# Kernel tuning notes

Hardware: AMD Instinct MI355X
Metric: run time of the kernel (lower is better)

## Reference

```python
import math
import jax, jax.numpy as jnp
import numpy as np

DIM = 512
HEADS = 8
LS = 64  # local_size
SCALE = (DIM // HEADS) ** -0.5


def _normalize(x, eps=1e-12):
    # torch F.normalize(dim=-1): x / max(||x||, eps)
    n = jnp.linalg.norm(x, axis=-1, keepdims=True)
    return x / jnp.maximum(n, eps)


def setup_inputs() -> dict:
    key = jax.random.key(0)
    k0, k1, k2 = jax.random.split(key, 3)
    B, S, D = 8, 4096, DIM
    return {
        "x": jax.random.normal(k0, (B, S, D), jnp.float32),
        "W_qkv": jax.random.normal(k1, (D, 3 * D), jnp.float32) * 0.02,
        "b_qkv": jnp.zeros((3 * D,), jnp.float32),
        "W_proj": jax.random.normal(k2, (D, D), jnp.float32) * 0.02,
        "b_proj": jnp.zeros((D,), jnp.float32),
    }


def reference(x, W_qkv, b_qkv, W_proj, b_proj):
    B, S, D = x.shape
    H = HEADS
    d = D // H
    ls = LS
    nl = S // ls
    ntimes = int(math.log2(nl))

    # qkv projection -> [3, B, H, S, d]
    qkv = (x @ W_qkv + b_qkv).reshape(B, S, 3, H, d).transpose(2, 0, 3, 1, 4)
    q_pre = qkv[0].reshape(B * H, S, d).transpose(0, 2, 1)  # [BH, d, S]

    q_idx_last = jnp.broadcast_to(jnp.arange(S)[None, :], (B * H, S))

    # recursive content-based bipartition (unrolled: ntimes is static)
    for _ in range(ntimes):
        bh, dd, n = q_pre.shape
        q_avg = q_pre.reshape(bh, dd, 2, n // 2).mean(-1)        # [bh, d, 2]
        q_avg = _normalize(q_avg.transpose(0, 2, 1))             # [bh, 2, d]
        q_norm = _normalize(q_pre.transpose(0, 2, 1))            # [bh, n, d]
        # squared euclidean distance [bh, n, 2]
        sq = (jnp.sum(q_norm ** 2, -1)[:, :, None]
              + jnp.sum(q_avg ** 2, -1)[:, None, :]
              - 2.0 * jnp.einsum('bnd,bcd->bnc', q_norm, q_avg))
        q_ratio = (sq[:, :, 0] + 1.0) / (sq[:, :, 1] + 1.0)
        q_idx = jnp.argsort(q_ratio, axis=-1)                    # [bh, n]
        q_idx_last = jnp.take_along_axis(q_idx_last, q_idx, axis=-1).reshape(bh * 2, n // 2)
        q_pre = jnp.take_along_axis(q_pre, q_idx[:, None, :], axis=-1)
        # 'b d (c n) -> (b c) d n' with c=2
        q_pre = q_pre.reshape(bh, dd, 2, n // 2).transpose(0, 2, 1, 3).reshape(bh * 2, dd, n // 2)

    q_idx = q_idx_last.reshape(B, H, S)
    q_idx_rev = jnp.argsort(q_idx, axis=-1)

    # gather qkv along token dim with routed permutation
    qkv_pre = jnp.take_along_axis(qkv, q_idx[None, :, :, :, None], axis=3)  # [3,B,H,S,d]
    # 'qkv b h (nl ls) d -> qkv (b nl) h ls d'
    qkv_pre = qkv_pre.reshape(3, B, H, nl, ls, d).transpose(0, 1, 3, 2, 4, 5).reshape(3, B * nl, H, ls, d)
    q, k, v = qkv_pre[0], qkv_pre[1], qkv_pre[2]

    # windowed diff-softmax-mul attention (softmax over head dim d)
    attn = jax.nn.softmax((q - k) * SCALE, axis=-1)
    out = attn * v                                               # [(B nl), H, ls, d]

    # '(b nl) h ls d -> b h d (nl ls)'
    out = out.reshape(B, nl, H, ls, d).transpose(0, 2, 4, 1, 3).reshape(B, H, d, S)
    out = jnp.take_along_axis(out, q_idx_rev[:, :, None, :], axis=-1)
    res = out.reshape(B, D, S).transpose(0, 2, 1)                # [B, S, D]
    res = res @ W_proj + b_proj
    return x + res
```

## Files before the change

kernel.cpp:

```cpp
#include <hip/hip_runtime.h>
#include <hip/hip_bf16.h>

typedef __bf16 bf16;
typedef __attribute__((ext_vector_type(8))) __bf16 bf16x8;
typedef __attribute__((ext_vector_type(4))) __bf16 bf16x4;
typedef __attribute__((ext_vector_type(4))) float f32x4;

#define M_TOK 32768
#define D_    512
#define N_QKV 1536
#define BK    64
#define SCALE_ 0.125f

#define AS1 __attribute__((address_space(1)))
#define AS3 __attribute__((address_space(3)))

__global__ __launch_bounds__(256) void cvt_bf16(const float* __restrict__ in,
                                                bf16* __restrict__ out, int n4) {
  int i = blockIdx.x * 256 + threadIdx.x;
  if (i >= n4) return;
  f32x4 v = ((const f32x4*)in)[i];
  bf16x4 o;
  o[0] = (bf16)v[0]; o[1] = (bf16)v[1]; o[2] = (bf16)v[2]; o[3] = (bf16)v[3];
  ((bf16x4*)out)[i] = o;
}

template <int PERM>
__global__ __launch_bounds__(256) void transpose_cvt(const float* __restrict__ in,
                                                     bf16* __restrict__ out,
                                                     int K, int N) {
  __shared__ float tile[32][33];
  int n0 = blockIdx.x * 32, k0 = blockIdx.y * 32;
  int tx = threadIdx.x, ty = threadIdx.y;
  for (int i = 0; i < 32; i += 8)
    tile[ty + i][tx] = in[(size_t)(k0 + ty + i) * N + n0 + tx];
  __syncthreads();
  for (int i = 0; i < 32; i += 8) {
    int n = n0 + ty + i;
    int np = n;
    if (PERM) {
      int qkv = n >> 9, h = (n & 511) >> 6, c = n & 63;
      np = h * 192 + (c >> 5) * 96 + qkv * 32 + (c & 31);
    }
    out[(size_t)np * K + k0 + tx] = (bf16)tile[tx][ty + i];
  }
}

__global__ __launch_bounds__(256, 2) void gemm_qkv_softmax(const bf16* __restrict__ A,
                                                           const bf16* __restrict__ Bt,
                                                           const float* __restrict__ bqkv,
                                                           bf16* __restrict__ O) {
  __shared__ __align__(16) bf16 sA[2][128 * BK];
  __shared__ __align__(16) bf16 sB[2][192 * BK];

  const int tid = threadIdx.x;
  const int w = tid >> 6;
  const int l = tid & 63;
  const int m0 = blockIdx.x * 128;
  const int h  = blockIdx.y;
  const int n0 = h * 192;
  const int wrow = w >> 1, wcol = w & 1;

  f32x4 acc[4][6];
#pragma unroll
  for (int i = 0; i < 4; ++i)
#pragma unroll
    for (int j = 0; j < 6; ++j) {
      f32x4 z = {0.f, 0.f, 0.f, 0.f};
      acc[i][j] = z;
    }

  const int srow = l >> 3;
  const int schunk = ((l & 7) ^ (l >> 3)) * 8;

  const int fr = l & 15;
  const int fkc = l >> 4;
  const int frs = fr & 7;

  const bf16* gA = A + (size_t)(m0 + w * 32 + srow) * D_ + schunk;
  const bf16* gB = Bt + (size_t)(n0 + w * 48 + srow) * D_ + schunk;

  auto stageA = [&](int buf, int kt) {
#pragma unroll
    for (int q = 0; q < 4; ++q)
      __builtin_amdgcn_global_load_lds((AS1 const void*)(gA + (size_t)(q * 8) * D_ + kt),
                                       (AS3 void*)&sA[buf][(w * 32 + q * 8) * BK], 16, 0, 0);
  };
  auto stageB = [&](int buf, int kt) {
#pragma unroll
    for (int q = 0; q < 6; ++q)
      __builtin_amdgcn_global_load_lds((AS1 const void*)(gB + (size_t)(q * 8) * D_ + kt),
                                       (AS3 void*)&sB[buf][(w * 48 + q * 8) * BK], 16, 0, 0);
  };

  auto compute = [&](int buf, int kk) {
    const int sw = (((kk << 2) | fkc) ^ frs) * 8;
    bf16x8 af[4], bfr[6];
#pragma unroll
    for (int i = 0; i < 4; ++i)
      af[i] = *(const bf16x8*)&sA[buf][(wrow * 64 + i * 16 + fr) * BK + sw];
#pragma unroll
    for (int j = 0; j < 6; ++j)
      bfr[j] = *(const bf16x8*)&sB[buf][(wcol * 96 + j * 16 + fr) * BK + sw];
    __builtin_amdgcn_s_setprio(1);
#pragma unroll
    for (int i = 0; i < 4; ++i)
#pragma unroll
      for (int j = 0; j < 6; ++j)
        acc[i][j] = __builtin_amdgcn_mfma_f32_16x16x32_bf16(af[i], bfr[j], acc[i][j], 0, 0, 0);
    __builtin_amdgcn_s_setprio(0);
  };

  stageA(0, 0);
  stageB(0, 0);

  const int NT = D_ / BK;
  for (int t = 0; t < NT - 1; ++t) {
    const int cur = t & 1;
    stageA(cur ^ 1, (t + 1) * BK);
    asm volatile("s_waitcnt vmcnt(4)" ::: "memory");
    __builtin_amdgcn_s_barrier();
    asm volatile("" ::: "memory");
    compute(cur, 0);
    stageB(cur ^ 1, (t + 1) * BK);
    compute(cur, 1);
    asm volatile("" ::: "memory");
    __builtin_amdgcn_s_barrier();
  }
  {
    const int cur = (NT - 1) & 1;
    asm volatile("s_waitcnt vmcnt(0)" ::: "memory");
    __builtin_amdgcn_s_barrier();
    asm volatile("" ::: "memory");
    compute(cur, 0);
    compute(cur, 1);
    asm volatile("" ::: "memory");
    __builtin_amdgcn_s_barrier();
  }

  float bq[2], bkk[2], bv[2];
#pragma unroll
  for (int jq = 0; jq < 2; ++jq) {
    int c = h * 64 + wcol * 32 + jq * 16 + fr;
    bq[jq]  = bqkv[c];
    bkk[jq] = bqkv[512 + c];
    bv[jq]  = bqkv[1024 + c];
  }

  float* xm = (float*)&sA[0][0];
  float* xs = xm + 256;
  const int rbase = (l >> 4) * 4;

  float mpart[4][4], spart[4][4];
#pragma unroll
  for (int i = 0; i < 4; ++i) {
#pragma unroll
    for (int r = 0; r < 4; ++r) {
      float s0 = (acc[i][0][r] + bq[0] - acc[i][2][r] - bkk[0]) * SCALE_;
      float s1 = (acc[i][1][r] + bq[1] - acc[i][3][r] - bkk[1]) * SCALE_;
      float mx = fmaxf(s0, s1);
#pragma unroll
      for (int off = 1; off < 16; off <<= 1) mx = fmaxf(mx, __shfl_xor(mx, off));
      float e0 = __expf(s0 - mx);
      float e1 = __expf(s1 - mx);
      acc[i][0][r] = e0;
      acc[i][1][r] = e1;
      float sm = e0 + e1;
#pragma unroll
      for (int off = 1; off < 16; off <<= 1) sm += __shfl_xor(sm, off);
      mpart[i][r] = mx;
      spart[i][r] = sm;
      if (fr == 0) {
        int row = wrow * 64 + i * 16 + rbase + r;
        xm[wcol * 128 + row] = mx;
        xs[wcol * 128 + row] = sm;
      }
    }
  }
  __syncthreads();

#pragma unroll
  for (int i = 0; i < 4; ++i) {
#pragma unroll
    for (int r = 0; r < 4; ++r) {
      int row = wrow * 64 + i * 16 + rbase + r;
      float mo = xm[(wcol ^ 1) * 128 + row];
      float so = xs[(wcol ^ 1) * 128 + row];
      float mx = mpart[i][r];
      float M  = fmaxf(mx, mo);
      float esc_self  = __expf(mx - M);
      float esc_other = __expf(mo - M);
      float total = spart[i][r] * esc_self + so * esc_other;
      float inv = esc_self / total;
      int m = m0 + row;
      float o0 = acc[i][0][r] * inv * (acc[i][4][r] + bv[0]);
      float o1 = acc[i][1][r] * inv * (acc[i][5][r] + bv[1]);
      O[(size_t)m * D_ + h * 64 + wcol * 32 + fr]      = (bf16)o0;
      O[(size_t)m * D_ + h * 64 + wcol * 32 + 16 + fr] = (bf16)o1;
    }
  }
}

__global__ __launch_bounds__(256, 2) void gemm_bt_f32(const bf16* __restrict__ A,
                                                      const bf16* __restrict__ Bt,
                                                      const float* __restrict__ bias,
                                                      const float* __restrict__ resid,
                                                      float* __restrict__ C,
                                                      int M, int N, int K) {
  __shared__ __align__(16) bf16 sA[2][128 * BK];
  __shared__ __align__(16) bf16 sB[2][128 * BK];

  const int tid = threadIdx.x;
  const int w = tid >> 6;
  const int l = tid & 63;
  const int m0 = blockIdx.x * 128;
  const int n0 = blockIdx.y * 128;
  const int wrow = w >> 1, wcol = w & 1;

  f32x4 acc[4][4];
#pragma unroll
  for (int i = 0; i < 4; ++i)
#pragma unroll
    for (int j = 0; j < 4; ++j) {
      f32x4 z = {0.f, 0.f, 0.f, 0.f};
      acc[i][j] = z;
    }

  const int srow = l >> 3;
  const int schunk = ((l & 7) ^ (l >> 3)) * 8;
  const int fr = l & 15;
  const int fkc = l >> 4;
  const int frs = fr & 7;

  const bf16* gA = A + (size_t)(m0 + w * 32 + srow) * K + schunk;
  const bf16* gB = Bt + (size_t)(n0 + w * 32 + srow) * K + schunk;

  auto stageA = [&](int buf, int kt) {
#pragma unroll
    for (int q = 0; q < 4; ++q)
      __builtin_amdgcn_global_load_lds((AS1 const void*)(gA + (size_t)(q * 8) * K + kt),
                                       (AS3 void*)&sA[buf][(w * 32 + q * 8) * BK], 16, 0, 0);
  };
  auto stageB = [&](int buf, int kt) {
#pragma unroll
    for (int q = 0; q < 4; ++q)
      __builtin_amdgcn_global_load_lds((AS1 const void*)(gB + (size_t)(q * 8) * K + kt),
                                       (AS3 void*)&sB[buf][(w * 32 + q * 8) * BK], 16, 0, 0);
  };

  auto compute = [&](int buf, int kk) {
    const int sw = (((kk << 2) | fkc) ^ frs) * 8;
    bf16x8 af[4], bfr[4];
#pragma unroll
    for (int i = 0; i < 4; ++i)
      af[i] = *(const bf16x8*)&sA[buf][(wrow * 64 + i * 16 + fr) * BK + sw];
#pragma unroll
    for (int j = 0; j < 4; ++j)
      bfr[j] = *(const bf16x8*)&sB[buf][(wcol * 64 + j * 16 + fr) * BK + sw];
    __builtin_amdgcn_s_setprio(1);
#pragma unroll
    for (int i = 0; i < 4; ++i)
#pragma unroll
      for (int j = 0; j < 4; ++j)
        acc[i][j] = __builtin_amdgcn_mfma_f32_16x16x32_bf16(af[i], bfr[j], acc[i][j], 0, 0, 0);
    __builtin_amdgcn_s_setprio(0);
  };

  stageA(0, 0);
  stageB(0, 0);

  const int nt = K / BK;
  for (int t = 0; t < nt - 1; ++t) {
    const int cur = t & 1;
    stageA(cur ^ 1, (t + 1) * BK);
    asm volatile("s_waitcnt vmcnt(4)" ::: "memory");
    __builtin_amdgcn_s_barrier();
    asm volatile("" ::: "memory");
    compute(cur, 0);
    stageB(cur ^ 1, (t + 1) * BK);
    compute(cur, 1);
    asm volatile("" ::: "memory");
    __builtin_amdgcn_s_barrier();
  }
  {
    const int cur = (nt - 1) & 1;
    asm volatile("s_waitcnt vmcnt(0)" ::: "memory");
    __builtin_amdgcn_s_barrier();
    asm volatile("" ::: "memory");
    compute(cur, 0);
    compute(cur, 1);
  }

  const int col = l & 15;
  const int rbase = (l >> 4) * 4;
#pragma unroll
  for (int j = 0; j < 4; ++j) {
    int n = n0 + wcol * 64 + j * 16 + col;
    float bv = bias[n];
#pragma unroll
    for (int i = 0; i < 4; ++i) {
#pragma unroll
      for (int r = 0; r < 4; ++r) {
        int m = m0 + wrow * 64 + i * 16 + rbase + r;
        C[(size_t)m * N + n] = acc[i][j][r] + bv + resid[(size_t)m * N + n];
      }
    }
  }
}

extern "C" void kernel_launch(void* const* d_in, const int* in_sizes, int n_in,
                              void* d_out, int out_size, void* d_ws, size_t ws_size,
                              hipStream_t stream) {
  const float* x     = (const float*)d_in[0];
  const float* Wqkv  = (const float*)d_in[1];
  const float* bqkv  = (const float*)d_in[2];
  const float* Wproj = (const float*)d_in[3];
  const float* bproj = (const float*)d_in[4];
  float* out = (float*)d_out;

  char* ws = (char*)d_ws;
  bf16* Wq_t = (bf16*)ws;
  bf16* Wp_t = (bf16*)(ws + (size_t)N_QKV * D_ * 2);
  char* p = ws + (size_t)N_QKV * D_ * 2 + (size_t)D_ * D_ * 2;
  bf16* Xb = (bf16*)p;
  bf16* O  = (bf16*)(p + (size_t)M_TOK * D_ * 2);

  transpose_cvt<1><<<dim3(N_QKV / 32, D_ / 32), dim3(32, 8), 0, stream>>>(Wqkv, Wq_t, D_, N_QKV);
  transpose_cvt<0><<<dim3(D_ / 32, D_ / 32), dim3(32, 8), 0, stream>>>(Wproj, Wp_t, D_, D_);

  cvt_bf16<<<(M_TOK * D_ / 4 + 255) / 256, 256, 0, stream>>>(x, Xb, M_TOK * D_ / 4);

  gemm_qkv_softmax<<<dim3(M_TOK / 128, 8), 256, 0, stream>>>(Xb, Wq_t, bqkv, O);

  gemm_bt_f32<<<dim3(M_TOK / 128, D_ / 128), 256, 0, stream>>>(
      O, Wp_t, bproj, x, out, M_TOK, D_, D_);
}
```

Measured before the change: 238.2 us.

## Enlarge QKV GEMM tile to 256 rows with 8 waves and triple-buffered A

The fused QKV+softmax GEMM now uses 512-thread blocks covering 256 token rows. The A operand is triple-buffered and B double-buffered, and the k-loop is rewritten into four phases per tile. Global-to-LDS prefetches are interleaved between MFMA groups, with explicit lgkmcnt waits and sched barriers. This aims to reuse each B tile across more rows and hide load latency better. In exchange it uses more LDS per block, which may reduce occupancy, and adds more barriers per k-step.

Measured after the change: 245.2 us. +2.9%, slower.

```diff
diff --git a/kernel.cpp b/kernel.cpp
--- a/kernel.cpp
+++ b/kernel.cpp
@@ -46,17 +46,17 @@
   }
 }
 
-__global__ __launch_bounds__(256, 2) void gemm_qkv_softmax(const bf16* __restrict__ A,
+__global__ __launch_bounds__(512, 2) void gemm_qkv_softmax(const bf16* __restrict__ A,
                                                            const bf16* __restrict__ Bt,
                                                            const float* __restrict__ bqkv,
                                                            bf16* __restrict__ O) {
-  __shared__ __align__(16) bf16 sA[2][128 * BK];
+  __shared__ __align__(16) bf16 sA[3][256 * BK];
   __shared__ __align__(16) bf16 sB[2][192 * BK];
 
   const int tid = threadIdx.x;
   const int w = tid >> 6;
   const int l = tid & 63;
-  const int m0 = blockIdx.x * 128;
+  const int m0 = blockIdx.x * 256;
   const int h  = blockIdx.y;
   const int n0 = h * 192;
   const int wrow = w >> 1, wcol = w & 1;
@@ -78,63 +78,95 @@
   const int frs = fr & 7;
 
   const bf16* gA = A + (size_t)(m0 + w * 32 + srow) * D_ + schunk;
-  const bf16* gB = Bt + (size_t)(n0 + w * 48 + srow) * D_ + schunk;
-
-  auto stageA = [&](int buf, int kt) {
-#pragma unroll
-    for (int q = 0; q < 4; ++q)
-      __builtin_amdgcn_global_load_lds((AS1 const void*)(gA + (size_t)(q * 8) * D_ + kt),
-                                       (AS3 void*)&sA[buf][(w * 32 + q * 8) * BK], 16, 0, 0);
-  };
-  auto stageB = [&](int buf, int kt) {
-#pragma unroll
-    for (int q = 0; q < 6; ++q)
-      __builtin_amdgcn_global_load_lds((AS1 const void*)(gB + (size_t)(q * 8) * D_ + kt),
-                                       (AS3 void*)&sB[buf][(w * 48 + q * 8) * BK], 16, 0, 0);
-  };
-
-  auto compute = [&](int buf, int kk) {
+  const bf16* gB = Bt + (size_t)(n0 + w * 24 + srow) * D_ + schunk;
+
+  auto stA = [&](int buf, int kt, int q) {
+    __builtin_amdgcn_global_load_lds((AS1 const void*)(gA + (size_t)(q * 8) * D_ + kt),
+                                     (AS3 void*)&sA[buf][(w * 32 + q * 8) * BK], 16, 0, 0);
+  };
+  auto stB = [&](int buf, int kt, int q) {
+    __builtin_amdgcn_global_load_lds((AS1 const void*)(gB + (size_t)(q * 8) * D_ + kt),
+                                     (AS3 void*)&sB[buf][(w * 24 + q * 8) * BK], 16, 0, 0);
+  };
+
+  bf16x8 af[4];
+  auto loadA = [&](int buf, int kk) {
     const int sw = (((kk << 2) | fkc) ^ frs) * 8;
-    bf16x8 af[4], bfr[6];
 #pragma unroll
     for (int i = 0; i < 4; ++i)
       af[i] = *(const bf16x8*)&sA[buf][(wrow * 64 + i * 16 + fr) * BK + sw];
-#pragma unroll
-    for (int j = 0; j < 6; ++j)
-      bfr[j] = *(const bf16x8*)&sB[buf][(wcol * 96 + j * 16 + fr) * BK + sw];
+  };
+  bf16x8 bfr[3];
+  auto loadB3 = [&](int buf, int kk, int jh) {
+    const int sw = (((kk << 2) | fkc) ^ frs) * 8;
+#pragma unroll
+    for (int j = 0; j < 3; ++j)
+      bfr[j] = *(const bf16x8*)&sB[buf][(wcol * 96 + (jh * 3 + j) * 16 + fr) * BK + sw];
+  };
+  auto mfma12 = [&](int jh) {
     __builtin_amdgcn_s_setprio(1);
 #pragma unroll
     for (int i = 0; i < 4; ++i)
 #pragma unroll
-      for (int j = 0; j < 6; ++j)
-        acc[i][j] = __builtin_amdgcn_mfma_f32_16x16x32_bf16(af[i], bfr[j], acc[i][j], 0, 0, 0);
+      for (int j = 0; j < 3; ++j)
+        acc[i][jh * 3 + j] =
+            __builtin_amdgcn_mfma_f32_16x16x32_bf16(af[i], bfr[j], acc[i][jh * 3 + j], 0, 0, 0);
     __builtin_amdgcn_s_setprio(0);
   };
 
-  stageA(0, 0);
-  stageB(0, 0);
+#pragma unroll
+  for (int q = 0; q < 4; ++q) stA(0, 0, q);
+#pragma unroll
+  for (int q = 0; q < 3; ++q) stB(0, 0, q);
+#pragma unroll
+  for (int q = 0; q < 4; ++q) stA(1, BK, q);
 
   const int NT = D_ / BK;
-  for (int t = 0; t < NT - 1; ++t) {
-    const int cur = t & 1;
-    stageA(cur ^ 1, (t + 1) * BK);
-    asm volatile("s_waitcnt vmcnt(4)" ::: "memory");
-    __builtin_amdgcn_s_barrier();
-    asm volatile("" ::: "memory");
-    compute(cur, 0);
-    stageB(cur ^ 1, (t + 1) * BK);
-    compute(cur, 1);
-    asm volatile("" ::: "memory");
-    __builtin_amdgcn_s_barrier();
-  }
-  {
-    const int cur = (NT - 1) & 1;
-    asm volatile("s_waitcnt vmcnt(0)" ::: "memory");
-    __builtin_amdgcn_s_barrier();
-    asm volatile("" ::: "memory");
-    compute(cur, 0);
-    compute(cur, 1);
-    asm volatile("" ::: "memory");
+#pragma unroll
+  for (int t = 0; t < NT; ++t) {
+    const int cA = t % 3;
+    const int cB = t & 1;
+    const int nA = (t + 2) % 3;
+    const int nB = cB ^ 1;
+    const int ktA = (t + 2) * BK;
+    const int ktB = (t + 1) * BK;
+    const bool pfA = (t < NT - 2);
+    const bool pfB = (t < NT - 1);
+
+    if (pfB) { stB(nB, ktB, 0); stB(nB, ktB, 1); }
+    if (t < NT - 1)
+      asm volatile("s_waitcnt vmcnt(6)" ::: "memory");
+    else
+      asm volatile("s_waitcnt vmcnt(0)" ::: "memory");
+    __builtin_amdgcn_s_barrier();
+    loadA(cA, 0);
+    loadB3(cB, 0, 0);
+    asm volatile("s_waitcnt lgkmcnt(0)" ::: "memory");
+    __builtin_amdgcn_sched_barrier(0);
+    mfma12(0);
+    __builtin_amdgcn_s_barrier();
+
+    loadB3(cB, 0, 1);
+    if (pfB) stB(nB, ktB, 2);
+    if (pfA) stA(nA, ktA, 0);
+    asm volatile("s_waitcnt lgkmcnt(0)" ::: "memory");
+    __builtin_amdgcn_sched_barrier(0);
+    mfma12(1);
+    __builtin_amdgcn_s_barrier();
+
+    loadA(cA, 1);
+    loadB3(cB, 1, 0);
+    if (pfA) { stA(nA, ktA, 1); stA(nA, ktA, 2); }
+    asm volatile("s_waitcnt lgkmcnt(0)" ::: "memory");
+    __builtin_amdgcn_sched_barrier(0);
+    mfma12(0);
+    __builtin_amdgcn_s_barrier();
+
+    loadB3(cB, 1, 1);
+    if (pfA) stA(nA, ktA, 3);
+    asm volatile("s_waitcnt lgkmcnt(0)" ::: "memory");
+    __builtin_amdgcn_sched_barrier(0);
+    mfma12(1);
     __builtin_amdgcn_s_barrier();
   }
 
@@ -148,7 +180,7 @@
   }
 
   float* xm = (float*)&sA[0][0];
-  float* xs = xm + 256;
+  float* xs = xm + 512;
   const int rbase = (l >> 4) * 4;
 
   float mpart[4][4], spart[4][4];
@@ -172,8 +204,8 @@
       spart[i][r] = sm;
       if (fr == 0) {
         int row = wrow * 64 + i * 16 + rbase + r;
-        xm[wcol * 128 + row] = mx;
-        xs[wcol * 128 + row] = sm;
+        xm[wcol * 256 + row] = mx;
+        xs[wcol * 256 + row] = sm;
       }
     }
   }
@@ -184,8 +216,8 @@
 #pragma unroll
     for (int r = 0; r < 4; ++r) {
       int row = wrow * 64 + i * 16 + rbase + r;
-      float mo = xm[(wcol ^ 1) * 128 + row];
-      float so = xs[(wcol ^ 1) * 128 + row];
+      float mo = xm[(wcol ^ 1) * 256 + row];
+      float so = xs[(wcol ^ 1) * 256 + row];
       float mx = mpart[i][r];
       float M  = fmaxf(mx, mo);
       float esc_self  = __expf(mx - M);
@@ -330,7 +362,7 @@
 
   cvt_bf16<<<(M_TOK * D_ / 4 + 255) / 256, 256, 0, stream>>>(x, Xb, M_TOK * D_ / 4);
 
-  gemm_qkv_softmax<<<dim3(M_TOK / 128, 8), 256, 0, stream>>>(Xb, Wq_t, bqkv, O);
+  gemm_qkv_softmax<<<dim3(M_TOK / 256, 8), 512, 0, stream>>>(Xb, Wq_t, bqkv, O);
 
   gemm_bt_f32<<<dim3(M_TOK / 128, D_ / 128), 256, 0, stream>>>(
       O, Wp_t, bproj, x, out, M_TOK, D_, D_);
```

## Fuse x fp32-to-bf16 conversion into QKV GEMM A-tile loading

Applied to the files above, without the earlier changes.

Removes the separate cvt_bf16 pass over x and has the QKV GEMM load fp32 x directly into registers, convert to bf16, and write it into swizzled LDS. The load/compute pipeline is restructured so next-tile A loads go to registers and B loads go straight to LDS, with the LDS write after compute. The two weight transpose kernels are merged into one launch. Cost: the GEMM reads x at twice the bytes, and the eight x tiles are re-read by each head block, so more HBM/L2 traffic and register pressure inside the GEMM.

New measurement: 229.6 us. 3.6% less time.

```diff
diff --git a/kernel.cpp b/kernel.cpp
--- a/kernel.cpp
+++ b/kernel.cpp
@@ -15,38 +15,35 @@
 #define AS1 __attribute__((address_space(1)))
 #define AS3 __attribute__((address_space(3)))
 
-__global__ __launch_bounds__(256) void cvt_bf16(const float* __restrict__ in,
-                                                bf16* __restrict__ out, int n4) {
-  int i = blockIdx.x * 256 + threadIdx.x;
-  if (i >= n4) return;
-  f32x4 v = ((const f32x4*)in)[i];
-  bf16x4 o;
-  o[0] = (bf16)v[0]; o[1] = (bf16)v[1]; o[2] = (bf16)v[2]; o[3] = (bf16)v[3];
-  ((bf16x4*)out)[i] = o;
-}
-
-template <int PERM>
-__global__ __launch_bounds__(256) void transpose_cvt(const float* __restrict__ in,
-                                                     bf16* __restrict__ out,
-                                                     int K, int N) {
+__global__ __launch_bounds__(256) void transpose_cvt_all(const float* __restrict__ Wqkv,
+                                                         const float* __restrict__ Wproj,
+                                                         bf16* __restrict__ Wq_t,
+                                                         bf16* __restrict__ Wp_t) {
   __shared__ float tile[32][33];
-  int n0 = blockIdx.x * 32, k0 = blockIdx.y * 32;
-  int tx = threadIdx.x, ty = threadIdx.y;
+  const int bx = blockIdx.x;
+  const float* in;
+  bf16* out;
+  int N, n0;
+  bool perm;
+  if (bx < 48) { in = Wqkv;  out = Wq_t; N = 1536; n0 = bx * 32;        perm = true;  }
+  else         { in = Wproj; out = Wp_t; N = 512;  n0 = (bx - 48) * 32; perm = false; }
+  const int k0 = blockIdx.y * 32;
+  const int tx = threadIdx.x, ty = threadIdx.y;
   for (int i = 0; i < 32; i += 8)
     tile[ty + i][tx] = in[(size_t)(k0 + ty + i) * N + n0 + tx];
   __syncthreads();
   for (int i = 0; i < 32; i += 8) {
     int n = n0 + ty + i;
     int np = n;
-    if (PERM) {
+    if (perm) {
       int qkv = n >> 9, h = (n & 511) >> 6, c = n & 63;
       np = h * 192 + (c >> 5) * 96 + qkv * 32 + (c & 31);
     }
-    out[(size_t)np * K + k0 + tx] = (bf16)tile[tx][ty + i];
+    out[(size_t)np * D_ + k0 + tx] = (bf16)tile[tx][ty + i];
   }
 }
 
-__global__ __launch_bounds__(256, 2) void gemm_qkv_softmax(const bf16* __restrict__ A,
+__global__ __launch_bounds__(256, 2) void gemm_qkv_softmax(const float* __restrict__ A,
                                                            const bf16* __restrict__ Bt,
                                                            const float* __restrict__ bqkv,
                                                            bf16* __restrict__ O) {
@@ -71,20 +68,31 @@
     }
 
   const int srow = l >> 3;
-  const int schunk = ((l & 7) ^ (l >> 3)) * 8;
-
+  const int schunk = ((l & 7) ^ srow) * 8;
   const int fr = l & 15;
   const int fkc = l >> 4;
   const int frs = fr & 7;
 
-  const bf16* gA = A + (size_t)(m0 + w * 32 + srow) * D_ + schunk;
-  const bf16* gB = Bt + (size_t)(n0 + w * 48 + srow) * D_ + schunk;
-
-  auto stageA = [&](int buf, int kt) {
-#pragma unroll
-    for (int q = 0; q < 4; ++q)
-      __builtin_amdgcn_global_load_lds((AS1 const void*)(gA + (size_t)(q * 8) * D_ + kt),
-                                       (AS3 void*)&sA[buf][(w * 32 + q * 8) * BK], 16, 0, 0);
+  const float* gA = A + (size_t)(m0 + w * 32 + srow) * D_ + (l & 7) * 8;
+  const bf16*  gB = Bt + (size_t)(n0 + w * 48 + srow) * D_ + schunk;
+
+  f32x4 areg[4][2];
+  auto aregLoad = [&](int kt) {
+#pragma unroll
+    for (int q = 0; q < 4; ++q) {
+      const float* gp = gA + (size_t)(q * 8) * D_ + kt;
+      areg[q][0] = *(const f32x4*)gp;
+      areg[q][1] = *(const f32x4*)(gp + 4);
+    }
+  };
+  auto aWrite = [&](int buf) {
+#pragma unroll
+    for (int q = 0; q < 4; ++q) {
+      bf16x8 v;
+#pragma unroll
+      for (int e = 0; e < 4; ++e) { v[e] = (bf16)areg[q][0][e]; v[4 + e] = (bf16)areg[q][1][e]; }
+      *(bf16x8*)&sA[buf][(w * 32 + q * 8 + srow) * BK + ((l & 7) ^ srow) * 8] = v;
+    }
   };
   auto stageB = [&](int buf, int kt) {
 #pragma unroll
@@ -111,29 +119,29 @@
     __builtin_amdgcn_s_setprio(0);
   };
 
-  stageA(0, 0);
+  aregLoad(0);
   stageB(0, 0);
+  aWrite(0);
+  asm volatile("s_waitcnt lgkmcnt(0)" ::: "memory");
 
   const int NT = D_ / BK;
-  for (int t = 0; t < NT - 1; ++t) {
+  for (int t = 0; t < NT; ++t) {
     const int cur = t & 1;
-    stageA(cur ^ 1, (t + 1) * BK);
-    asm volatile("s_waitcnt vmcnt(4)" ::: "memory");
-    __builtin_amdgcn_s_barrier();
-    asm volatile("" ::: "memory");
-    compute(cur, 0);
-    stageB(cur ^ 1, (t + 1) * BK);
-    compute(cur, 1);
-    asm volatile("" ::: "memory");
-    __builtin_amdgcn_s_barrier();
-  }
-  {
-    const int cur = (NT - 1) & 1;
-    asm volatile("s_waitcnt vmcnt(0)" ::: "memory");
+    if (t < NT - 1) {
+      aregLoad((t + 1) * BK);
+      stageB(cur ^ 1, (t + 1) * BK);
+      asm volatile("s_waitcnt vmcnt(14)" ::: "memory");
+    } else {
+      asm volatile("s_waitcnt vmcnt(0)" ::: "memory");
+    }
     __builtin_amdgcn_s_barrier();
     asm volatile("" ::: "memory");
     compute(cur, 0);
     compute(cur, 1);
+    if (t < NT - 1) {
+      aWrite(cur ^ 1);
+      asm volatile("s_waitcnt lgkmcnt(0)" ::: "memory");
+    }
     asm volatile("" ::: "memory");
     __builtin_amdgcn_s_barrier();
   }
@@ -321,16 +329,11 @@
   char* ws = (char*)d_ws;
   bf16* Wq_t = (bf16*)ws;
   bf16* Wp_t = (bf16*)(ws + (size_t)N_QKV * D_ * 2);
-  char* p = ws + (size_t)N_QKV * D_ * 2 + (size_t)D_ * D_ * 2;
-  bf16* Xb = (bf16*)p;
-  bf16* O  = (bf16*)(p + (size_t)M_TOK * D_ * 2);
-
-  transpose_cvt<1><<<dim3(N_QKV / 32, D_ / 32), dim3(32, 8), 0, stream>>>(Wqkv, Wq_t, D_, N_QKV);
-  transpose_cvt<0><<<dim3(D_ / 32, D_ / 32), dim3(32, 8), 0, stream>>>(Wproj, Wp_t, D_, D_);
-
-  cvt_bf16<<<(M_TOK * D_ / 4 + 255) / 256, 256, 0, stream>>>(x, Xb, M_TOK * D_ / 4);
-
-  gemm_qkv_softmax<<<dim3(M_TOK / 128, 8), 256, 0, stream>>>(Xb, Wq_t, bqkv, O);
+  bf16* O    = (bf16*)(ws + (size_t)N_QKV * D_ * 2 + (size_t)D_ * D_ * 2);
+
+  transpose_cvt_all<<<dim3(64, 16), dim3(32, 8), 0, stream>>>(Wqkv, Wproj, Wq_t, Wp_t);
+
+  gemm_qkv_softmax<<<dim3(M_TOK / 128, 8), 256, 0, stream>>>(x, Wq_t, bqkv, O);
 
   gemm_bt_f32<<<dim3(M_TOK / 128, D_ / 128), 256, 0, stream>>>(
       O, Wp_t, bproj, x, out, M_TOK, D_, D_);
```
